# Kernel tuning notes

Measured on AMD Instinct MI355X. Metric: run time of the kernel, lower is better.

Reference implementation:

```python
import jax, jax.numpy as jnp
import numpy as np

N, H, W = 1024, 256, 256
EPS2D = 0.3  # gsplat low-pass filter on 2D covariance

C0 = 0.28209479177387814
C1 = 0.4886025119029199
C2 = (1.0925484305920792, -1.0925484305920792, 0.31539156525252005, -1.0925484305920792, 0.5462742152960396)
C3 = (-0.5900435899266435, 2.890611442640554, -0.4570457994644658, 0.3731763325901154, -0.4570457994644658, 1.445305721320277, -0.5900435899266435)


def setup_inputs() -> dict:
    key = jax.random.key(0)
    ks = jax.random.split(key, 9)
    means = jax.random.normal(ks[0], (N, 3), jnp.float32)
    scales = jax.random.normal(ks[1], (N, 3), jnp.float32) * 0.3 - 3.0  # exp -> ~0.05
    quats = jax.random.normal(ks[2], (N, 4), jnp.float32)
    opacities = jax.random.normal(ks[3], (N, 1), jnp.float32)
    sh_0 = jax.random.normal(ks[4], (N, 1, 3), jnp.float32) * 0.5
    sh_n = jax.random.normal(ks[5], (N, 15, 3), jnp.float32) * 0.1
    times = jax.random.uniform(ks[6], (N, 1), jnp.float32)
    durations = jax.random.normal(ks[7], (N, 1), jnp.float32) * 0.5
    velocities = jax.random.normal(ks[8], (N, 3), jnp.float32) * 0.1
    # camera: identity rotation, points pushed to depth ~5 in front
    w2c = jnp.eye(4, dtype=jnp.float32).at[2, 3].set(5.0)[None]
    intrinsic = jnp.array([[[300.0, 0.0, 128.0], [0.0, 300.0, 128.0], [0.0, 0.0, 1.0]]], jnp.float32)
    return {"means": means, "scales": scales, "quats": quats, "opacities": opacities,
            "sh_0": sh_0, "sh_n": sh_n, "times": times, "durations": durations,
            "velocities": velocities, "t": jnp.float32(0.5), "w2c": w2c,
            "intrinsic": intrinsic, "height": H, "width": W}


def _quat_to_rot(q):
    q = q / jnp.linalg.norm(q, axis=-1, keepdims=True)
    w, x, y, z = q[:, 0], q[:, 1], q[:, 2], q[:, 3]
    R = jnp.stack([
        1 - 2 * (y * y + z * z), 2 * (x * y - w * z), 2 * (x * z + w * y),
        2 * (x * y + w * z), 1 - 2 * (x * x + z * z), 2 * (y * z - w * x),
        2 * (x * z - w * y), 2 * (y * z + w * x), 1 - 2 * (x * x + y * y),
    ], axis=-1).reshape(-1, 3, 3)
    return R


def _sh_colors(sh, dirs):
    # sh: [N,16,3], dirs: [N,3] normalized. Real SH up to degree 3 (gsplat convention).
    x, y, z = dirs[:, 0], dirs[:, 1], dirs[:, 2]
    xx, yy, zz = x * x, y * y, z * z
    basis = jnp.stack([
        jnp.full_like(x, C0),
        -C1 * y, C1 * z, -C1 * x,
        C2[0] * x * y, C2[1] * y * z, C2[2] * (2 * zz - xx - yy), C2[3] * x * z, C2[4] * (xx - yy),
        C3[0] * y * (3 * xx - yy), C3[1] * x * y * z, C3[2] * y * (4 * zz - xx - yy),
        C3[3] * z * (2 * zz - 3 * xx - 3 * yy), C3[4] * x * (4 * zz - xx - yy),
        C3[5] * z * (xx - yy), C3[6] * x * (xx - 3 * yy),
    ], axis=-1)  # [N,16]
    return jnp.maximum(jnp.einsum('nk,nkc->nc', basis, sh) + 0.5, 0.0)


def reference(means, scales, quats, opacities, sh_0, sh_n, times, durations, velocities,
              t, w2c, intrinsic, height, width):
    # temporal updates
    means_t = means + (t - times) * velocities                                   # [N,3]
    opac = (jax.nn.sigmoid(opacities) * jnp.exp(-0.5 * ((t - times) / jnp.exp(durations)) ** 2))[:, 0]
    sig = jnp.exp(scales)                                                        # [N,3]

    Rcw, tcw = w2c[0, :3, :3], w2c[0, :3, 3]
    K = intrinsic[0]
    fx, fy, cx, cy = K[0, 0], K[1, 1], K[0, 2], K[1, 2]

    # project means
    p_cam = means_t @ Rcw.T + tcw                                                # [N,3]
    zc = p_cam[:, 2]
    u = fx * p_cam[:, 0] / zc + cx
    v = fy * p_cam[:, 1] / zc + cy

    # 3D covariance in camera frame
    Rg = _quat_to_rot(quats)                                                     # [N,3,3]
    M = Rg * sig[:, None, :]
    cov3d = jnp.einsum('nij,nkj->nik', M, M)
    cov_cam = jnp.einsum('ij,njk,lk->nil', Rcw, cov3d, Rcw)

    # perspective Jacobian -> 2D covariance (EWA)
    zero = jnp.zeros_like(zc)
    J = jnp.stack([
        jnp.stack([fx / zc, zero, -fx * p_cam[:, 0] / zc ** 2], -1),
        jnp.stack([zero, fy / zc, -fy * p_cam[:, 1] / zc ** 2], -1),
    ], axis=1)                                                                   # [N,2,3]
    cov2d = jnp.einsum('nij,njk,nlk->nil', J, cov_cam, J)
    a = cov2d[:, 0, 0] + EPS2D
    b = cov2d[:, 0, 1]
    c = cov2d[:, 1, 1] + EPS2D
    det = a * c - b * b
    conA, conB, conC = c / det, -b / det, a / det

    # colors from SH
    cam_pos = -Rcw.T @ tcw
    dirs = means_t - cam_pos
    dirs = dirs / jnp.linalg.norm(dirs, axis=-1, keepdims=True)
    colors = _sh_colors(jnp.concatenate([sh_0, sh_n], axis=1), dirs)             # [N,3]

    # dense per-pixel gaussian evaluation (pixel centers at +0.5)
    xs = jnp.arange(width, dtype=jnp.float32) + 0.5
    ys = jnp.arange(height, dtype=jnp.float32) + 0.5
    gx, gy = jnp.meshgrid(xs, ys)                                                # [H,W]
    px, py = gx.reshape(-1), gy.reshape(-1)                                      # [HW]
    dx = px[None, :] - u[:, None]                                                # [N,HW]
    dy = py[None, :] - v[:, None]
    sigma = 0.5 * (conA[:, None] * dx * dx + conC[:, None] * dy * dy) + conB[:, None] * dx * dy
    valid = (zc > 0.01) & (det > 1e-12)
    alpha = jnp.minimum(0.999, opac[:, None] * jnp.exp(-jnp.maximum(sigma, 0.0)))
    alpha = jnp.where(valid[:, None] & (sigma >= 0.0) & (alpha >= 1.0 / 255.0), alpha, 0.0)

    # depth sort, front-to-back alpha compositing
    order = jnp.argsort(zc)
    alpha_s = alpha[order]
    colors_s = colors[order]
    Tcum = jnp.cumprod(1.0 - alpha_s, axis=0)                                    # [N,HW]
    T_excl = jnp.concatenate([jnp.ones((1, alpha_s.shape[1]), alpha_s.dtype), Tcum[:-1]], axis=0)
    w = alpha_s * T_excl                                                         # [N,HW]
    image = jnp.einsum('np,nc->pc', w, colors_s).reshape(1, height, width, 3)
    alpha_out = (1.0 - Tcum[-1]).reshape(1, height, width, 1)
    image = jnp.clip(image, 0.0, 1.0)
    return image, alpha_out
```

## Files before the change

### kernel.cpp

```cpp
#include <hip/hip_runtime.h>
#include <math.h>

#define NG 1024
#define IH 256
#define IW 256
#define NPIX (IH*IW)

__global__ __launch_bounds__(64) void k_pre(
    const float* __restrict__ means, const float* __restrict__ scales,
    const float* __restrict__ quats, const float* __restrict__ opacs,
    const float* __restrict__ sh0, const float* __restrict__ shn,
    const float* __restrict__ times, const float* __restrict__ durs,
    const float* __restrict__ vels, const float* __restrict__ tptr,
    const float* __restrict__ w2c, const float* __restrict__ intr,
    float* __restrict__ zc_out, float* __restrict__ raw)
{
    int g = blockIdx.x * 64 + threadIdx.x;
    if (g >= NG) return;
    const float t = tptr[0];
    const float R00=w2c[0], R01=w2c[1], R02=w2c[2],  tx=w2c[3];
    const float R10=w2c[4], R11=w2c[5], R12=w2c[6],  ty=w2c[7];
    const float R20=w2c[8], R21=w2c[9], R22=w2c[10], tz=w2c[11];
    const float fx=intr[0], cx=intr[2], fy=intr[4], cy=intr[5];

    const float dt = t - times[g];
    const float mx = fmaf(dt, vels[g*3+0], means[g*3+0]);
    const float my = fmaf(dt, vels[g*3+1], means[g*3+1]);
    const float mz = fmaf(dt, vels[g*3+2], means[g*3+2]);

    const float o = opacs[g];
    const float sig_o = 1.f / (1.f + __expf(-o));
    const float ratio = dt * __expf(-durs[g]);
    const float opac = sig_o * __expf(-0.5f * ratio * ratio);

    const float xc = R00*mx + R01*my + R02*mz + tx;
    const float yc = R10*mx + R11*my + R12*mz + ty;
    const float zc = R20*mx + R21*my + R22*mz + tz;
    const float iz = 1.f / zc;
    const float u = fx*xc*iz + cx;
    const float v = fy*yc*iz + cy;

    float qw=quats[g*4+0], qx=quats[g*4+1], qy=quats[g*4+2], qz=quats[g*4+3];
    const float qn = rsqrtf(qw*qw + qx*qx + qy*qy + qz*qz);
    qw*=qn; qx*=qn; qy*=qn; qz*=qn;
    const float sx = __expf(scales[g*3+0]);
    const float sy = __expf(scales[g*3+1]);
    const float sz = __expf(scales[g*3+2]);
    const float G00 = 1.f-2.f*(qy*qy+qz*qz), G01 = 2.f*(qx*qy-qw*qz), G02 = 2.f*(qx*qz+qw*qy);
    const float G10 = 2.f*(qx*qy+qw*qz), G11 = 1.f-2.f*(qx*qx+qz*qz), G12 = 2.f*(qy*qz-qw*qx);
    const float G20 = 2.f*(qx*qz-qw*qy), G21 = 2.f*(qy*qz+qw*qx), G22 = 1.f-2.f*(qx*qx+qy*qy);
    const float M00=G00*sx, M01=G01*sy, M02=G02*sz;
    const float M10=G10*sx, M11=G11*sy, M12=G12*sz;
    const float M20=G20*sx, M21=G21*sy, M22=G22*sz;
    const float W00=R00*M00+R01*M10+R02*M20, W01=R00*M01+R01*M11+R02*M21, W02=R00*M02+R01*M12+R02*M22;
    const float W10=R10*M00+R11*M10+R12*M20, W11=R10*M01+R11*M11+R12*M21, W12=R10*M02+R11*M12+R12*M22;
    const float W20=R20*M00+R21*M10+R22*M20, W21=R20*M01+R21*M11+R22*M21, W22=R20*M02+R21*M12+R22*M22;
    const float xdz = xc*iz, ydz = yc*iz;
    const float fxiz = fx*iz, fyiz = fy*iz;
    const float T00 = fxiz*(W00 - xdz*W20), T01 = fxiz*(W01 - xdz*W21), T02 = fxiz*(W02 - xdz*W22);
    const float T10 = fyiz*(W10 - ydz*W20), T11 = fyiz*(W11 - ydz*W21), T12 = fyiz*(W12 - ydz*W22);
    const float a = T00*T00 + T01*T01 + T02*T02 + 0.3f;
    const float b = T00*T10 + T01*T11 + T02*T12;
    const float c = T10*T10 + T11*T11 + T12*T12 + 0.3f;
    const float det = a*c - b*b;
    const float idet = 1.f / det;
    const float conA = c*idet, conB = -b*idet, conC = a*idet;

    const bool valid = (zc > 0.01f) && (det > 1e-12f);
    const float op_eff = valid ? opac : 0.f;
    const float smax = (op_eff * 255.f > 0.f) ? (logf(op_eff * 255.f) + 1e-4f) : -1e30f;
    float rx, ry;
    if (smax > 0.f) {
        rx = sqrtf(2.f * smax * a) + 0.01f;
        ry = sqrtf(2.f * smax * c) + 0.01f;
    } else {
        rx = -1e30f; ry = -1e30f;
    }

    const float cpx = -(R00*tx + R10*ty + R20*tz);
    const float cpy = -(R01*tx + R11*ty + R21*tz);
    const float cpz = -(R02*tx + R12*ty + R22*tz);
    float dx0 = mx-cpx, dy0 = my-cpy, dz0 = mz-cpz;
    const float dn = rsqrtf(dx0*dx0 + dy0*dy0 + dz0*dz0);
    const float X = dx0*dn, Y = dy0*dn, Z = dz0*dn;
    const float XX=X*X, YY=Y*Y, ZZ=Z*Z;

    float bs[16];
    bs[0]  = 0.28209479177387814f;
    bs[1]  = -0.4886025119029199f * Y;
    bs[2]  =  0.4886025119029199f * Z;
    bs[3]  = -0.4886025119029199f * X;
    bs[4]  =  1.0925484305920792f * X * Y;
    bs[5]  = -1.0925484305920792f * Y * Z;
    bs[6]  =  0.31539156525252005f * (2.f*ZZ - XX - YY);
    bs[7]  = -1.0925484305920792f * X * Z;
    bs[8]  =  0.5462742152960396f * (XX - YY);
    bs[9]  = -0.5900435899266435f * Y * (3.f*XX - YY);
    bs[10] =  2.890611442640554f  * X * Y * Z;
    bs[11] = -0.4570457994644658f * Y * (4.f*ZZ - XX - YY);
    bs[12] =  0.3731763325901154f * Z * (2.f*ZZ - 3.f*XX - 3.f*YY);
    bs[13] = -0.4570457994644658f * X * (4.f*ZZ - XX - YY);
    bs[14] =  1.445305721320277f  * Z * (XX - YY);
    bs[15] = -0.5900435899266435f * X * (XX - 3.f*YY);

    float cr = 0.5f, cg = 0.5f, cb = 0.5f;
    cr = fmaf(bs[0], sh0[g*3+0], cr);
    cg = fmaf(bs[0], sh0[g*3+1], cg);
    cb = fmaf(bs[0], sh0[g*3+2], cb);
    #pragma unroll
    for (int k = 1; k < 16; ++k) {
        const float* s = shn + g*45 + (k-1)*3;
        cr = fmaf(bs[k], s[0], cr);
        cg = fmaf(bs[k], s[1], cg);
        cb = fmaf(bs[k], s[2], cb);
    }
    cr = fmaxf(cr, 0.f); cg = fmaxf(cg, 0.f); cb = fmaxf(cb, 0.f);

    zc_out[g] = zc;
    float* r = raw + g*12;
    r[0] = u;            r[1] = v;      r[2] = 0.5f*conA; r[3] = conB;
    r[4] = 0.5f*conC;    r[5] = op_eff; r[6] = smax;      r[7] = cr;
    r[8] = cg;           r[9] = cb;     r[10] = rx;       r[11] = ry;
}

__global__ __launch_bounds__(64) void k_rank(
    const float* __restrict__ zc, const float* __restrict__ raw,
    float* __restrict__ sorted)
{
    const int g = blockIdx.x;
    const int lane = threadIdx.x;
    const float myz = zc[g];
    int cnt = 0;
    #pragma unroll
    for (int k = 0; k < 16; ++k) {
        const int j = k*64 + lane;
        const float z = zc[j];
        const bool lt = (z < myz) || (z == myz && j < g);
        cnt += (int)__popcll(__ballot(lt));
    }
    if (lane < 12) sorted[cnt*12 + lane] = raw[g*12 + lane];
}

__global__ __launch_bounds__(256) void k_raster(
    const float* __restrict__ sorted, float* __restrict__ out)
{
    __shared__ float4 lds[4][64];
    const int lane = threadIdx.x & 63;
    const int wv   = threadIdx.x >> 6;
    const int pix  = blockIdx.x * 64 + lane;
    const float px = (float)(pix & (IW-1)) + 0.5f;
    const float py = (float)(pix >> 8) + 0.5f;
    const float px0  = (float)((blockIdx.x & 3) * 64) + 0.5f;
    const float px63 = px0 + 63.f;

    const float4* __restrict__ gp = (const float4*)sorted;
    const int base = __builtin_amdgcn_readfirstlane(wv) * 256;

    unsigned long long mask0, mask1, mask2, mask3;
    {
        const int g0 = base + lane;
        const float4 a0 = gp[(g0      )*3 + 0];
        const float4 c0 = gp[(g0      )*3 + 2];
        const float4 a1 = gp[(g0 +  64)*3 + 0];
        const float4 c1 = gp[(g0 +  64)*3 + 2];
        const float4 a2 = gp[(g0 + 128)*3 + 0];
        const float4 c2 = gp[(g0 + 128)*3 + 2];
        const float4 a3 = gp[(g0 + 192)*3 + 0];
        const float4 c3 = gp[(g0 + 192)*3 + 2];
        mask0 = __ballot((fabsf(py - a0.y) <= c0.w) && (a0.x + c0.z >= px0) && (a0.x - c0.z <= px63));
        mask1 = __ballot((fabsf(py - a1.y) <= c1.w) && (a1.x + c1.z >= px0) && (a1.x - c1.z <= px63));
        mask2 = __ballot((fabsf(py - a2.y) <= c2.w) && (a2.x + c2.z >= px0) && (a2.x - c2.z <= px63));
        mask3 = __ballot((fabsf(py - a3.y) <= c3.w) && (a3.x + c3.z >= px0) && (a3.x - c3.z <= px63));
    }

    float T = 1.f, cr = 0.f, cg = 0.f, cb = 0.f;
    #pragma unroll
    for (int k = 0; k < 4; ++k) {
        unsigned long long m = (k==0) ? mask0 : (k==1) ? mask1 : (k==2) ? mask2 : mask3;
        const int kb = base + k*64;
        while (m) {
            const int b = __builtin_ctzll(m);
            m &= m - 1;
            const int g = kb + b;
            const float4 pa = gp[g*3+0];
            const float4 pb = gp[g*3+1];
            const float4 pc = gp[g*3+2];
            const float dx = px - pa.x;
            const float dy = py - pa.y;
            const float s1 = pa.z*dx + pa.w*dy;
            const float sigma = fmaf(dx, s1, pb.x*dy*dy);
            if (sigma >= 0.f && sigma <= pb.z) {
                const float al = fminf(0.999f, pb.y * __expf(-sigma));
                if (al >= (1.f/255.f)) {
                    const float w = al * T;
                    cr = fmaf(w, pb.w, cr);
                    cg = fmaf(w, pc.x, cg);
                    cb = fmaf(w, pc.y, cb);
                    T -= w;
                }
            }
        }
    }

    lds[wv][lane] = make_float4(cr, cg, cb, T);
    __syncthreads();
    if (threadIdx.x < 64) {
        const float4 v0 = lds[0][lane];
        const float4 v1 = lds[1][lane];
        const float4 v2 = lds[2][lane];
        const float4 v3 = lds[3][lane];
        float r = v0.x, g2 = v0.y, b2 = v0.z, Tt = v0.w;
        r = fmaf(Tt, v1.x, r); g2 = fmaf(Tt, v1.y, g2); b2 = fmaf(Tt, v1.z, b2); Tt *= v1.w;
        r = fmaf(Tt, v2.x, r); g2 = fmaf(Tt, v2.y, g2); b2 = fmaf(Tt, v2.z, b2); Tt *= v2.w;
        r = fmaf(Tt, v3.x, r); g2 = fmaf(Tt, v3.y, g2); b2 = fmaf(Tt, v3.z, b2); Tt *= v3.w;
        const int p3 = pix * 3;
        out[p3+0] = fminf(fmaxf(r,  0.f), 1.f);
        out[p3+1] = fminf(fmaxf(g2, 0.f), 1.f);
        out[p3+2] = fminf(fmaxf(b2, 0.f), 1.f);
        out[NPIX*3 + pix] = 1.f - Tt;
    }
}

extern "C" void kernel_launch(void* const* d_in, const int* in_sizes, int n_in,
                              void* d_out, int out_size, void* d_ws, size_t ws_size,
                              hipStream_t stream) {
    const float* means  = (const float*)d_in[0];
    const float* scales = (const float*)d_in[1];
    const float* quats  = (const float*)d_in[2];
    const float* opacs  = (const float*)d_in[3];
    const float* sh0    = (const float*)d_in[4];
    const float* shn    = (const float*)d_in[5];
    const float* times  = (const float*)d_in[6];
    const float* durs   = (const float*)d_in[7];
    const float* vels   = (const float*)d_in[8];
    const float* tptr   = (const float*)d_in[9];
    const float* w2c    = (const float*)d_in[10];
    const float* intr   = (const float*)d_in[11];

    float* ws     = (float*)d_ws;
    float* zc     = ws;
    float* raw    = ws + 1024;
    float* sorted = ws + 1024 + 12*NG;

    hipLaunchKernelGGL(k_pre, dim3(16), dim3(64), 0, stream,
                       means, scales, quats, opacs, sh0, shn,
                       times, durs, vels, tptr, w2c, intr, zc, raw);
    hipLaunchKernelGGL(k_rank, dim3(NG), dim3(64), 0, stream, zc, raw, sorted);
    hipLaunchKernelGGL(k_raster, dim3(NPIX/64), dim3(256), 0, stream,
                       sorted, (float*)d_out);
}
```

Measured before the change: 20.46 us.

## Compact per-wave hit Gaussians into LDS and repack records for single-load culling

The per-Gaussian record is reordered so the culling fields (u, v, rx, ry) sit in the first float4, so the culling test needs one vector load instead of two. Each wave then writes the records of its hit Gaussians, compacted by popcount position, into a per-wave LDS buffer. All lanes then iterate over that buffer instead of issuing scattered global loads per set bit. This replaces serial dependent global/L2 loads with cooperative coalesced loads plus LDS broadcast reads. It relies on an explicit lgkmcnt wait rather than a barrier, and adds LDS usage that may affect occupancy.

```diff
diff --git a/kernel.cpp b/kernel.cpp
--- a/kernel.cpp
+++ b/kernel.cpp
@@ -5,6 +5,7 @@
 #define IH 256
 #define IW 256
 #define NPIX (IH*IW)
+
 
 __global__ __launch_bounds__(64) void k_pre(
     const float* __restrict__ means, const float* __restrict__ scales,
@@ -118,9 +119,9 @@
 
     zc_out[g] = zc;
     float* r = raw + g*12;
-    r[0] = u;            r[1] = v;      r[2] = 0.5f*conA; r[3] = conB;
-    r[4] = 0.5f*conC;    r[5] = op_eff; r[6] = smax;      r[7] = cr;
-    r[8] = cg;           r[9] = cb;     r[10] = rx;       r[11] = ry;
+    r[0] = u;         r[1] = v;    r[2]  = rx;       r[3]  = ry;
+    r[4] = 0.5f*conA; r[5] = conB; r[6]  = 0.5f*conC;r[7]  = smax;
+    r[8] = op_eff;    r[9] = cr;   r[10] = cg;       r[11] = cb;
 }
 
 __global__ __launch_bounds__(64) void k_rank(
@@ -144,71 +145,68 @@
 __global__ __launch_bounds__(256) void k_raster(
     const float* __restrict__ sorted, float* __restrict__ out)
 {
-    __shared__ float4 lds[4][64];
+    __shared__ float4 hrec[4][64][3];
+    __shared__ float4 part[4][64];
     const int lane = threadIdx.x & 63;
     const int wv   = threadIdx.x >> 6;
     const int pix  = blockIdx.x * 64 + lane;
     const float px = (float)(pix & (IW-1)) + 0.5f;
     const float py = (float)(pix >> 8) + 0.5f;
-    const float px0  = (float)((blockIdx.x & 3) * 64) + 0.5f;
+    const float px0  = (float)((blockIdx.x & 3) << 6) + 0.5f;
     const float px63 = px0 + 63.f;
 
     const float4* __restrict__ gp = (const float4*)sorted;
-    const int base = __builtin_amdgcn_readfirstlane(wv) * 256;
-
-    unsigned long long mask0, mask1, mask2, mask3;
-    {
-        const int g0 = base + lane;
-        const float4 a0 = gp[(g0      )*3 + 0];
-        const float4 c0 = gp[(g0      )*3 + 2];
-        const float4 a1 = gp[(g0 +  64)*3 + 0];
-        const float4 c1 = gp[(g0 +  64)*3 + 2];
-        const float4 a2 = gp[(g0 + 128)*3 + 0];
-        const float4 c2 = gp[(g0 + 128)*3 + 2];
-        const float4 a3 = gp[(g0 + 192)*3 + 0];
-        const float4 c3 = gp[(g0 + 192)*3 + 2];
-        mask0 = __ballot((fabsf(py - a0.y) <= c0.w) && (a0.x + c0.z >= px0) && (a0.x - c0.z <= px63));
-        mask1 = __ballot((fabsf(py - a1.y) <= c1.w) && (a1.x + c1.z >= px0) && (a1.x - c1.z <= px63));
-        mask2 = __ballot((fabsf(py - a2.y) <= c2.w) && (a2.x + c2.z >= px0) && (a2.x - c2.z <= px63));
-        mask3 = __ballot((fabsf(py - a3.y) <= c3.w) && (a3.x + c3.z >= px0) && (a3.x - c3.z <= px63));
+    const int base = wv * 256;
+
+    unsigned long long masks[4];
+    #pragma unroll
+    for (int k = 0; k < 4; ++k) {
+        const float4 r0 = gp[(base + k*64 + lane)*3];
+        masks[k] = __ballot((fabsf(py - r0.y) <= r0.w) &&
+                            (r0.x + r0.z >= px0) && (r0.x - r0.z <= px63));
     }
 
     float T = 1.f, cr = 0.f, cg = 0.f, cb = 0.f;
     #pragma unroll
     for (int k = 0; k < 4; ++k) {
-        unsigned long long m = (k==0) ? mask0 : (k==1) ? mask1 : (k==2) ? mask2 : mask3;
-        const int kb = base + k*64;
-        while (m) {
-            const int b = __builtin_ctzll(m);
-            m &= m - 1;
-            const int g = kb + b;
-            const float4 pa = gp[g*3+0];
-            const float4 pb = gp[g*3+1];
-            const float4 pc = gp[g*3+2];
-            const float dx = px - pa.x;
-            const float dy = py - pa.y;
-            const float s1 = pa.z*dx + pa.w*dy;
-            const float sigma = fmaf(dx, s1, pb.x*dy*dy);
-            if (sigma >= 0.f && sigma <= pb.z) {
-                const float al = fminf(0.999f, pb.y * __expf(-sigma));
+        const unsigned long long m = masks[k];
+        if (!m) continue;
+        const int g = base + k*64 + lane;
+        if ((m >> lane) & 1ull) {
+            const int pos = (int)__popcll(m & ((1ull << lane) - 1ull));
+            hrec[wv][pos][0] = gp[g*3+0];
+            hrec[wv][pos][1] = gp[g*3+1];
+            hrec[wv][pos][2] = gp[g*3+2];
+        }
+        asm volatile("s_waitcnt lgkmcnt(0)" ::: "memory");
+        const int cnt = (int)__popcll(m);
+        for (int i = 0; i < cnt; ++i) {
+            const float4 ra = hrec[wv][i][0];
+            const float4 rb = hrec[wv][i][1];
+            const float4 rc = hrec[wv][i][2];
+            const float dx = px - ra.x;
+            const float dy = py - ra.y;
+            const float sigma = fmaf(dx, fmaf(rb.x, dx, rb.y*dy), rb.z*dy*dy);
+            if (sigma >= 0.f && sigma <= rb.w) {
+                const float al = fminf(0.999f, rc.x * __expf(-sigma));
                 if (al >= (1.f/255.f)) {
                     const float w = al * T;
-                    cr = fmaf(w, pb.w, cr);
-                    cg = fmaf(w, pc.x, cg);
-                    cb = fmaf(w, pc.y, cb);
+                    cr = fmaf(w, rc.y, cr);
+                    cg = fmaf(w, rc.z, cg);
+                    cb = fmaf(w, rc.w, cb);
                     T -= w;
                 }
             }
         }
     }
 
-    lds[wv][lane] = make_float4(cr, cg, cb, T);
+    part[wv][lane] = make_float4(cr, cg, cb, T);
     __syncthreads();
     if (threadIdx.x < 64) {
-        const float4 v0 = lds[0][lane];
-        const float4 v1 = lds[1][lane];
-        const float4 v2 = lds[2][lane];
-        const float4 v3 = lds[3][lane];
+        const float4 v0 = part[0][lane];
+        const float4 v1 = part[1][lane];
+        const float4 v2 = part[2][lane];
+        const float4 v3 = part[3][lane];
         float r = v0.x, g2 = v0.y, b2 = v0.z, Tt = v0.w;
         r = fmaf(Tt, v1.x, r); g2 = fmaf(Tt, v1.y, g2); b2 = fmaf(Tt, v1.z, b2); Tt *= v1.w;
         r = fmaf(Tt, v2.x, r); g2 = fmaf(Tt, v2.y, g2); b2 = fmaf(Tt, v2.z, b2); Tt *= v2.w;
```

New measurement: 19.94 us. 2.5% less time.
